# Kernel tuning notes

Hardware: AMD Instinct MI355X
Metric: run time of the kernel (lower is better)

The kernel has to match this reference:

```python
import jax, jax.numpy as jnp
import numpy as np

H = 51  # num_hidden

def lstm_cell(x, h, c, Wih, Whh, bih, bhh):
    # PyTorch LSTMCell gate order: i, f, g, o
    gates = x @ Wih.T + bih + h @ Whh.T + bhh
    i, f, g, o = jnp.split(gates, 4, axis=-1)
    c_new = jax.nn.sigmoid(f) * c + jax.nn.sigmoid(i) * jnp.tanh(g)
    h_new = jax.nn.sigmoid(o) * jnp.tanh(c_new)
    return h_new, c_new

def setup_inputs() -> dict:
    key = jax.random.key(0)
    ks = jax.random.split(key, 9)
    B, T = 8192, 512
    s1 = 1.0 / np.sqrt(H)  # torch LSTMCell init scale U(-1/sqrt(H), 1/sqrt(H))
    s2 = 1.0
    u = lambda k, shape, s: jax.random.uniform(k, shape, jnp.float32, -s, s)
    return {
        "x": jax.random.normal(ks[0], (B, T), dtype=jnp.float32),
        "Wih1": u(ks[1], (4 * H, 1), s1),
        "Whh1": u(ks[2], (4 * H, H), s1),
        "bih1": u(ks[3], (4 * H,), s1),
        "bhh1": u(ks[4], (4 * H,), s1),
        "Wih2": u(ks[5], (4, H), s2),
        "Whh2": u(ks[6], (4, 1), s2),
        "bih2": u(ks[7], (4,), s2),
        "bhh2": u(ks[8], (4,), s2),
    }

def reference(x, Wih1, Whh1, bih1, bhh1, Wih2, Whh2, bih2, bhh2):
    B, T = x.shape
    xs = x.T[:, :, None]  # [T, B, 1]
    h1 = jnp.zeros((B, H), x.dtype)
    c1 = jnp.zeros((B, H), x.dtype)
    h2 = jnp.zeros((B, 1), x.dtype)
    c2 = jnp.zeros((B, 1), x.dtype)

    def step(carry, xt):
        h1, c1, h2, c2 = carry
        h1, c1 = lstm_cell(xt, h1, c1, Wih1, Whh1, bih1, bhh1)
        h2, c2 = lstm_cell(c1, h2, c2, Wih2, Whh2, bih2, bhh2)
        return (h1, c1, h2, c2), None

    (h1, c1, h2, c2), _ = jax.lax.scan(step, (h1, c1, h2, c2), xs)
    # extra step after the loop (as in the original forward)
    h1, c1 = lstm_cell(c2, h1, c1, Wih1, Whh1, bih1, bhh1)
    h2, output = lstm_cell(c1, h2, c2, Wih2, Whh2, bih2, bhh2)
    return output  # [B, 1] (final cell state of lstm2)
```

## Files before the change

kernel.cpp:

```cpp
#include <hip/hip_runtime.h>

#define TT 512

typedef _Float16 f16;
typedef _Float16 f16x4 __attribute__((ext_vector_type(4)));
typedef _Float16 f16x8 __attribute__((ext_vector_type(8)));
typedef float f32x4 __attribute__((ext_vector_type(4)));

__device__ __forceinline__ float fsig(float x){
    return __builtin_amdgcn_rcpf(1.f + __expf(-x));
}
__device__ __forceinline__ float ftanh_(float x){
    return 2.f * __builtin_amdgcn_rcpf(1.f + __expf(-2.f*x)) - 1.f;
}

#define FMA_LO(accv, wd, hh) asm("v_fma_mix_f32 %0, %1, %2, %0 op_sel:[0,0,0] op_sel_hi:[1,0,0]" : "+v"(accv) : "v"(wd), "v"(hh))
#define FMA_HI(accv, wd, hh) asm("v_fma_mix_f32 %0, %1, %2, %0 op_sel:[1,0,0] op_sel_hi:[1,0,0]" : "+v"(accv) : "v"(wd), "v"(hh))

__global__ void repack_w(const float* __restrict__ Whh1, const float* __restrict__ Wih1,
                         const float* __restrict__ bih1, const float* __restrict__ bhh1,
                         const float* __restrict__ Wih2,
                         f16* __restrict__ Wp, f16* __restrict__ Wp2)
{
    int i = blockIdx.x*256 + threadIdx.x;
    if (i < 13*2*64*8) {
        int b    = i & 7;
        int lane = (i >> 3) & 63;
        int kt   = (i >> 9) & 1;
        int m    = i >> 10;
        int r = m*16 + (lane & 15);
        int u = r >> 2, g = r & 3;
        int k = kt*32 + (lane >> 4)*8 + b;
        float v = 0.f;
        if (u < 51) {
            int rt = g*51 + u;
            if      (k < 51)  v = Whh1[rt*51 + k];
            else if (k == 51) v = Wih1[rt];
            else if (k == 52) v = bih1[rt] + bhh1[rt];
        }
        Wp[i] = (f16)v;
    }
    if (i < 224) {
        int u = i >> 2, g = i & 3;
        Wp2[i] = (f16)((u < 51) ? Wih2[g*51 + u] : 0.f);
    }
}

__global__ __launch_bounds__(256, 2) void lstm_main(
    const float* __restrict__ X, const f16* __restrict__ Wp, const f16* __restrict__ Wp2,
    const float* __restrict__ Whh2, const float* __restrict__ bih2, const float* __restrict__ bhh2,
    float* __restrict__ out)
{
    __shared__ __align__(16) f16   HB[1024];
    __shared__ __align__(16) float PBL[4][16][4];

    const int tid  = threadIdx.x;
    const int w    = tid >> 6;
    const int lane = tid & 63;
    const int q    = (lane >> 4) & 3;
    const int jl   = lane & 15;
    const int s    = jl << 2;
    const int bb   = blockIdx.x * 16;

    for (int i = tid; i < 512; i += 256) ((unsigned*)HB)[i] = 0u;
    {
        int i = tid;
        if (i < 256) ((unsigned*)PBL)[i] = 0u;
    }
    __syncthreads();
    if (w == 0 && lane < 16) {
        int ss = lane << 2;
        HB[lane*64 + (52 ^ ss)] = (f16)1.f;
        HB[lane*64 + (51 ^ ss)] = (f16)X[(size_t)(bb + lane)*TT];
    }

    const bool has4 = (w == 1);
    const int tiles[4] = {w, 4+w, 8+w, 12};
    f16x8 A0[4], A1[4];
    uint2 w2p[4];
    #pragma unroll
    for (int k = 0; k < 4; ++k) {
        int m = tiles[k];
        A0[k]  = *(const f16x8*)(Wp + (m*2+0)*512 + lane*8);
        A1[k]  = *(const f16x8*)(Wp + (m*2+1)*512 + lane*8);
        w2p[k] = *(const uint2*)(Wp2 + (m*4+q)*4);
    }
    float wh2[4], bs2[4];
    #pragma unroll
    for (int g = 0; g < 4; ++g) { wh2[g] = Whh2[g]; bs2[g] = bih2[g] + bhh2[g]; }

    float c1[4] = {0.f, 0.f, 0.f, 0.f};
    float c2 = 0.f, h2 = 0.f;
    const f32x4 zero4 = {0.f, 0.f, 0.f, 0.f};

    const float* xp = X + (size_t)(bb + jl) * TT;
    __syncthreads();

    for (int t = 0; t < TT; ++t) {
        const f16* rb = HB + jl*64;
        f16x4 b0lo = *(const f16x4*)(rb + (((q*8)     ) ^ s));
        f16x4 b0hi = *(const f16x4*)(rb + (((q*8) | 4 ) ^ s));
        f16x4 b1lo = *(const f16x4*)(rb + (((q*8) + 32) ^ s));
        f16x4 b1hi = *(const f16x4*)(rb + (((q*8) + 36) ^ s));
        f16x8 B0 = __builtin_shufflevector(b0lo, b0hi, 0,1,2,3,4,5,6,7);
        f16x8 B1 = __builtin_shufflevector(b1lo, b1hi, 0,1,2,3,4,5,6,7);

        f32x4 S0, S1, S2, S3;
        if (w == 3) {
            S0 = *(const f32x4*)&PBL[0][jl][0];
            S1 = *(const f32x4*)&PBL[1][jl][0];
            S2 = *(const f32x4*)&PBL[2][jl][0];
            S3 = *(const f32x4*)&PBL[3][jl][0];
        }
        float xn = xp[(t+1 < TT) ? t+1 : t];

        __syncthreads();

        if (w == 3 && t > 0) {
            f32x4 S = S0 + S1 + S2 + S3;
            float g0 = S[0] + bs2[0] + wh2[0]*h2;
            float g1 = S[1] + bs2[1] + wh2[1]*h2;
            float g2 = S[2] + bs2[2] + wh2[2]*h2;
            float g3 = S[3] + bs2[3] + wh2[3]*h2;
            float i2 = fsig(g0), f2 = fsig(g1), gg2 = ftanh_(g2), o2 = fsig(g3);
            c2 = f2*c2 + i2*gg2;
            h2 = o2*ftanh_(c2);
        }

        float p0 = 0.f, p1 = 0.f, p2 = 0.f, p3 = 0.f;
        #pragma unroll
        for (int k = 0; k < 4; ++k) {
            if (k < 3 || has4) {
                f32x4 a = __builtin_amdgcn_mfma_f32_16x16x32_f16(A0[k], B0, zero4, 0,0,0);
                a       = __builtin_amdgcn_mfma_f32_16x16x32_f16(A1[k], B1, a,     0,0,0);
                float ig = fsig(a[0]), fg = fsig(a[1]), gg = ftanh_(a[2]), og = fsig(a[3]);
                float c  = fg*c1[k] + ig*gg;
                c1[k] = c;
                int u = tiles[k]*4 + q;
                if (k < 3 || q < 3)
                    HB[jl*64 + (u ^ s)] = (f16)(og * ftanh_(c));
                FMA_LO(p0, w2p[k].x, c); FMA_HI(p1, w2p[k].x, c);
                FMA_LO(p2, w2p[k].y, c); FMA_HI(p3, w2p[k].y, c);
            }
        }
        if (w == 0 && q == 3)
            HB[jl*64 + (51 ^ s)] = (f16)xn;

        p0 += __shfl_xor(p0, 16); p0 += __shfl_xor(p0, 32);
        p1 += __shfl_xor(p1, 16); p1 += __shfl_xor(p1, 32);
        p2 += __shfl_xor(p2, 16); p2 += __shfl_xor(p2, 32);
        p3 += __shfl_xor(p3, 16); p3 += __shfl_xor(p3, 32);
        if (lane < 16) {
            f32x4 pv = {p0, p1, p2, p3};
            *(f32x4*)&PBL[w][jl][0] = pv;
        }
        __syncthreads();
    }

    if (w == 3) {
        f32x4 S = *(const f32x4*)&PBL[0][jl][0];
        S += *(const f32x4*)&PBL[1][jl][0];
        S += *(const f32x4*)&PBL[2][jl][0];
        S += *(const f32x4*)&PBL[3][jl][0];
        float g0 = S[0] + bs2[0] + wh2[0]*h2;
        float g1 = S[1] + bs2[1] + wh2[1]*h2;
        float g2 = S[2] + bs2[2] + wh2[2]*h2;
        float g3 = S[3] + bs2[3] + wh2[3]*h2;
        float i2 = fsig(g0), f2 = fsig(g1), gg2 = ftanh_(g2), o2 = fsig(g3);
        c2 = f2*c2 + i2*gg2;
        h2 = o2*ftanh_(c2);
        if (lane < 16) HB[jl*64 + (51 ^ s)] = (f16)c2;
    }
    __syncthreads();

    {
        const f16* rb = HB + jl*64;
        f16x4 b0lo = *(const f16x4*)(rb + (((q*8)     ) ^ s));
        f16x4 b0hi = *(const f16x4*)(rb + (((q*8) | 4 ) ^ s));
        f16x4 b1lo = *(const f16x4*)(rb + (((q*8) + 32) ^ s));
        f16x4 b1hi = *(const f16x4*)(rb + (((q*8) + 36) ^ s));
        f16x8 B0 = __builtin_shufflevector(b0lo, b0hi, 0,1,2,3,4,5,6,7);
        f16x8 B1 = __builtin_shufflevector(b1lo, b1hi, 0,1,2,3,4,5,6,7);

        float p0 = 0.f, p1 = 0.f, p2 = 0.f, p3 = 0.f;
        #pragma unroll
        for (int k = 0; k < 4; ++k) {
            if (k < 3 || has4) {
                f32x4 a = __builtin_amdgcn_mfma_f32_16x16x32_f16(A0[k], B0, zero4, 0,0,0);
                a       = __builtin_amdgcn_mfma_f32_16x16x32_f16(A1[k], B1, a,     0,0,0);
                float ig = fsig(a[0]), fg = fsig(a[1]), gg = ftanh_(a[2]);
                float c  = fg*c1[k] + ig*gg;
                FMA_LO(p0, w2p[k].x, c); FMA_HI(p1, w2p[k].x, c);
                FMA_LO(p2, w2p[k].y, c); FMA_HI(p3, w2p[k].y, c);
            }
        }
        p0 += __shfl_xor(p0, 16); p0 += __shfl_xor(p0, 32);
        p1 += __shfl_xor(p1, 16); p1 += __shfl_xor(p1, 32);
        p2 += __shfl_xor(p2, 16); p2 += __shfl_xor(p2, 32);
        p3 += __shfl_xor(p3, 16); p3 += __shfl_xor(p3, 32);
        if (lane < 16) {
            f32x4 pv = {p0, p1, p2, p3};
            *(f32x4*)&PBL[w][jl][0] = pv;
        }
    }
    __syncthreads();

    if (w == 3) {
        f32x4 S = *(const f32x4*)&PBL[0][jl][0];
        S += *(const f32x4*)&PBL[1][jl][0];
        S += *(const f32x4*)&PBL[2][jl][0];
        S += *(const f32x4*)&PBL[3][jl][0];
        float g0 = S[0] + bs2[0] + wh2[0]*h2;
        float g1 = S[1] + bs2[1] + wh2[1]*h2;
        float g2 = S[2] + bs2[2] + wh2[2]*h2;
        float i2 = fsig(g0), f2 = fsig(g1), gg2 = ftanh_(g2);
        float c2n = f2*c2 + i2*gg2;
        if (lane < 16) out[bb + jl] = c2n;
    }
}

extern "C" void kernel_launch(void* const* d_in, const int* in_sizes, int n_in,
                              void* d_out, int out_size, void* d_ws, size_t ws_size,
                              hipStream_t stream) {
    const float* X    = (const float*)d_in[0];
    const float* Wih1 = (const float*)d_in[1];
    const float* Whh1 = (const float*)d_in[2];
    const float* bih1 = (const float*)d_in[3];
    const float* bhh1 = (const float*)d_in[4];
    const float* Wih2 = (const float*)d_in[5];
    const float* Whh2 = (const float*)d_in[6];
    const float* bih2 = (const float*)d_in[7];
    const float* bhh2 = (const float*)d_in[8];
    float* out = (float*)d_out;

    f16* Wp  = (f16*)d_ws;
    f16* Wp2 = (f16*)((char*)d_ws + 26624);

    repack_w<<<52, 256, 0, stream>>>(Whh1, Wih1, bih1, bhh1, Wih2, Wp, Wp2);
    lstm_main<<<512, 256, 0, stream>>>(X, Wp, Wp2, Whh2, bih2, bhh2, out);
}
```

Baseline: 451.2 us.

## Prescale weights by log2e, use 16-byte LDS swizzle, prioritize critical waves

Folds the log2(e) factors (doubled for tanh gate rows) into the repacked layer-1 and layer-2 weights and biases, so gate activations can call exp2 directly with no multiply per element. Changes the hidden-state LDS swizzle from a 4-element XOR to an 8-element block XOR, so each B operand is read with one 16-byte load instead of two 8-byte loads and a shuffle. Raises scheduling priority for waves 1 and 3, which carry the extra tile and the layer-2 update, and limits the per-step x prefetch to wave 0. Scaling weights before the fp16 conversion changes rounding slightly, and the new swizzle must keep the x and bias slots consistent.

```diff
diff --git a/kernel.cpp b/kernel.cpp
--- a/kernel.cpp
+++ b/kernel.cpp
@@ -1,17 +1,21 @@
 #include <hip/hip_runtime.h>
 
 #define TT 512
+#define L2E  1.4426950408889634f
+#define L2E2 2.8853900817779268f
 
 typedef _Float16 f16;
-typedef _Float16 f16x4 __attribute__((ext_vector_type(4)));
 typedef _Float16 f16x8 __attribute__((ext_vector_type(8)));
 typedef float f32x4 __attribute__((ext_vector_type(4)));
 
-__device__ __forceinline__ float fsig(float x){
-    return __builtin_amdgcn_rcpf(1.f + __expf(-x));
-}
-__device__ __forceinline__ float ftanh_(float x){
-    return 2.f * __builtin_amdgcn_rcpf(1.f + __expf(-2.f*x)) - 1.f;
+__device__ __forceinline__ float fsig_p(float a){
+    return __builtin_amdgcn_rcpf(1.f + __builtin_amdgcn_exp2f(-a));
+}
+__device__ __forceinline__ float ftanhg_p(float a){
+    return 2.f * __builtin_amdgcn_rcpf(1.f + __builtin_amdgcn_exp2f(-a)) - 1.f;
+}
+__device__ __forceinline__ float ftanh_c(float c){
+    return 2.f * __builtin_amdgcn_rcpf(1.f + __builtin_amdgcn_exp2f(-L2E2*c)) - 1.f;
 }
 
 #define FMA_LO(accv, wd, hh) asm("v_fma_mix_f32 %0, %1, %2, %0 op_sel:[0,0,0] op_sel_hi:[1,0,0]" : "+v"(accv) : "v"(wd), "v"(hh))
@@ -37,12 +41,15 @@
             if      (k < 51)  v = Whh1[rt*51 + k];
             else if (k == 51) v = Wih1[rt];
             else if (k == 52) v = bih1[rt] + bhh1[rt];
+            v *= (g == 2) ? L2E2 : L2E;
         }
         Wp[i] = (f16)v;
     }
     if (i < 224) {
         int u = i >> 2, g = i & 3;
-        Wp2[i] = (f16)((u < 51) ? Wih2[g*51 + u] : 0.f);
+        float v = (u < 51) ? Wih2[g*51 + u] : 0.f;
+        v *= (g == 2) ? L2E2 : L2E;
+        Wp2[i] = (f16)v;
     }
 }
 
@@ -59,19 +66,18 @@
     const int lane = tid & 63;
     const int q    = (lane >> 4) & 3;
     const int jl   = lane & 15;
-    const int s    = jl << 2;
+    const int d8   = jl & 7;
     const int bb   = blockIdx.x * 16;
 
+    if (w == 1 || w == 3) __builtin_amdgcn_s_setprio(1);
+
     for (int i = tid; i < 512; i += 256) ((unsigned*)HB)[i] = 0u;
-    {
-        int i = tid;
-        if (i < 256) ((unsigned*)PBL)[i] = 0u;
-    }
+    if (tid < 256) ((unsigned*)PBL)[tid] = 0u;
     __syncthreads();
     if (w == 0 && lane < 16) {
-        int ss = lane << 2;
-        HB[lane*64 + (52 ^ ss)] = (f16)1.f;
-        HB[lane*64 + (51 ^ ss)] = (f16)X[(size_t)(bb + lane)*TT];
+        int dd = lane & 7;
+        HB[lane*64 + ((6 ^ dd) << 3) + 4] = (f16)1.f;
+        HB[lane*64 + ((6 ^ dd) << 3) + 3] = (f16)X[(size_t)(bb + lane)*TT];
     }
 
     const bool has4 = (w == 1);
@@ -87,7 +93,11 @@
     }
     float wh2[4], bs2[4];
     #pragma unroll
-    for (int g = 0; g < 4; ++g) { wh2[g] = Whh2[g]; bs2[g] = bih2[g] + bhh2[g]; }
+    for (int g = 0; g < 4; ++g) {
+        float sc = (g == 2) ? L2E2 : L2E;
+        wh2[g] = Whh2[g] * sc;
+        bs2[g] = (bih2[g] + bhh2[g]) * sc;
+    }
 
     float c1[4] = {0.f, 0.f, 0.f, 0.f};
     float c2 = 0.f, h2 = 0.f;
@@ -98,12 +108,8 @@
 
     for (int t = 0; t < TT; ++t) {
         const f16* rb = HB + jl*64;
-        f16x4 b0lo = *(const f16x4*)(rb + (((q*8)     ) ^ s));
-        f16x4 b0hi = *(const f16x4*)(rb + (((q*8) | 4 ) ^ s));
-        f16x4 b1lo = *(const f16x4*)(rb + (((q*8) + 32) ^ s));
-        f16x4 b1hi = *(const f16x4*)(rb + (((q*8) + 36) ^ s));
-        f16x8 B0 = __builtin_shufflevector(b0lo, b0hi, 0,1,2,3,4,5,6,7);
-        f16x8 B1 = __builtin_shufflevector(b1lo, b1hi, 0,1,2,3,4,5,6,7);
+        f16x8 B0 = *(const f16x8*)(rb + ((q       ^ d8) << 3));
+        f16x8 B1 = *(const f16x8*)(rb + (((4 + q) ^ d8) << 3));
 
         f32x4 S0, S1, S2, S3;
         if (w == 3) {
@@ -112,7 +118,8 @@
             S2 = *(const f32x4*)&PBL[2][jl][0];
             S3 = *(const f32x4*)&PBL[3][jl][0];
         }
-        float xn = xp[(t+1 < TT) ? t+1 : t];
+        float xn = 0.f;
+        if (w == 0) xn = xp[(t+1 < TT) ? t+1 : t];
 
         __syncthreads();
 
@@ -122,9 +129,9 @@
             float g1 = S[1] + bs2[1] + wh2[1]*h2;
             float g2 = S[2] + bs2[2] + wh2[2]*h2;
             float g3 = S[3] + bs2[3] + wh2[3]*h2;
-            float i2 = fsig(g0), f2 = fsig(g1), gg2 = ftanh_(g2), o2 = fsig(g3);
+            float i2 = fsig_p(g0), f2 = fsig_p(g1), gg2 = ftanhg_p(g2), o2 = fsig_p(g3);
             c2 = f2*c2 + i2*gg2;
-            h2 = o2*ftanh_(c2);
+            h2 = o2*ftanh_c(c2);
         }
 
         float p0 = 0.f, p1 = 0.f, p2 = 0.f, p3 = 0.f;
@@ -133,18 +140,18 @@
             if (k < 3 || has4) {
                 f32x4 a = __builtin_amdgcn_mfma_f32_16x16x32_f16(A0[k], B0, zero4, 0,0,0);
                 a       = __builtin_amdgcn_mfma_f32_16x16x32_f16(A1[k], B1, a,     0,0,0);
-                float ig = fsig(a[0]), fg = fsig(a[1]), gg = ftanh_(a[2]), og = fsig(a[3]);
+                float ig = fsig_p(a[0]), fg = fsig_p(a[1]), gg = ftanhg_p(a[2]), og = fsig_p(a[3]);
                 float c  = fg*c1[k] + ig*gg;
                 c1[k] = c;
                 int u = tiles[k]*4 + q;
                 if (k < 3 || q < 3)
-                    HB[jl*64 + (u ^ s)] = (f16)(og * ftanh_(c));
+                    HB[jl*64 + (((u >> 3) ^ d8) << 3) + (u & 7)] = (f16)(og * ftanh_c(c));
                 FMA_LO(p0, w2p[k].x, c); FMA_HI(p1, w2p[k].x, c);
                 FMA_LO(p2, w2p[k].y, c); FMA_HI(p3, w2p[k].y, c);
             }
         }
         if (w == 0 && q == 3)
-            HB[jl*64 + (51 ^ s)] = (f16)xn;
+            HB[jl*64 + ((6 ^ d8) << 3) + 3] = (f16)xn;
 
         p0 += __shfl_xor(p0, 16); p0 += __shfl_xor(p0, 32);
         p1 += __shfl_xor(p1, 16); p1 += __shfl_xor(p1, 32);
@@ -166,21 +173,17 @@
         float g1 = S[1] + bs2[1] + wh2[1]*h2;
         float g2 = S[2] + bs2[2] + wh2[2]*h2;
         float g3 = S[3] + bs2[3] + wh2[3]*h2;
-        float i2 = fsig(g0), f2 = fsig(g1), gg2 = ftanh_(g2), o2 = fsig(g3);
+        float i2 = fsig_p(g0), f2 = fsig_p(g1), gg2 = ftanhg_p(g2), o2 = fsig_p(g3);
         c2 = f2*c2 + i2*gg2;
-        h2 = o2*ftanh_(c2);
-        if (lane < 16) HB[jl*64 + (51 ^ s)] = (f16)c2;
+        h2 = o2*ftanh_c(c2);
+        if (lane < 16) HB[jl*64 + ((6 ^ d8) << 3) + 3] = (f16)c2;
     }
     __syncthreads();
 
     {
         const f16* rb = HB + jl*64;
-        f16x4 b0lo = *(const f16x4*)(rb + (((q*8)     ) ^ s));
-        f16x4 b0hi = *(const f16x4*)(rb + (((q*8) | 4 ) ^ s));
-        f16x4 b1lo = *(const f16x4*)(rb + (((q*8) + 32) ^ s));
-        f16x4 b1hi = *(const f16x4*)(rb + (((q*8) + 36) ^ s));
-        f16x8 B0 = __builtin_shufflevector(b0lo, b0hi, 0,1,2,3,4,5,6,7);
-        f16x8 B1 = __builtin_shufflevector(b1lo, b1hi, 0,1,2,3,4,5,6,7);
+        f16x8 B0 = *(const f16x8*)(rb + ((q       ^ d8) << 3));
+        f16x8 B1 = *(const f16x8*)(rb + (((4 + q) ^ d8) << 3));
 
         float p0 = 0.f, p1 = 0.f, p2 = 0.f, p3 = 0.f;
         #pragma unroll
@@ -188,7 +191,7 @@
             if (k < 3 || has4) {
                 f32x4 a = __builtin_amdgcn_mfma_f32_16x16x32_f16(A0[k], B0, zero4, 0,0,0);
                 a       = __builtin_amdgcn_mfma_f32_16x16x32_f16(A1[k], B1, a,     0,0,0);
-                float ig = fsig(a[0]), fg = fsig(a[1]), gg = ftanh_(a[2]);
+                float ig = fsig_p(a[0]), fg = fsig_p(a[1]), gg = ftanhg_p(a[2]);
                 float c  = fg*c1[k] + ig*gg;
                 FMA_LO(p0, w2p[k].x, c); FMA_HI(p1, w2p[k].x, c);
                 FMA_LO(p2, w2p[k].y, c); FMA_HI(p3, w2p[k].y, c);
@@ -213,7 +216,7 @@
         float g0 = S[0] + bs2[0] + wh2[0]*h2;
         float g1 = S[1] + bs2[1] + wh2[1]*h2;
         float g2 = S[2] + bs2[2] + wh2[2]*h2;
-        float i2 = fsig(g0), f2 = fsig(g1), gg2 = ftanh_(g2);
+        float i2 = fsig_p(g0), f2 = fsig_p(g1), gg2 = ftanhg_p(g2);
         float c2n = f2*c2 + i2*gg2;
         if (lane < 16) out[bb + jl] = c2n;
     }
```

Result: slower. 461.3 us (+2.2%).
